# Kernel optimization log

Measured on AMD Instinct MI355X. Metric: run time of the kernel, lower is better.

Reference implementation:

```python
import jax, jax.numpy as jnp
import numpy as np

D_STATE = 16


def setup_inputs() -> dict:
    key = jax.random.key(0)
    ks = jax.random.split(key, 7)
    B, S, D = 8, 4096, 64
    ds = D_STATE
    x = jax.random.normal(ks[0], (B, S, D), dtype=jnp.float32)
    # Selection layers modeled as Linear(d_model, out). W_A scaled small so the
    # random transition matrices are contractive over 4096 steps.
    W_A = jax.random.normal(ks[1], (D, ds * ds), dtype=jnp.float32) * 0.01
    b_A = jnp.zeros((ds * ds,), dtype=jnp.float32)
    W_B = jax.random.normal(ks[2], (D, ds * D), dtype=jnp.float32) * 0.05
    b_B = jnp.zeros((ds * D,), dtype=jnp.float32)
    W_C = jax.random.normal(ks[3], (D, ds * D), dtype=jnp.float32) * 0.05
    b_C = jnp.zeros((ds * D,), dtype=jnp.float32)
    return {"x": x, "W_A": W_A, "b_A": b_A, "W_B": W_B, "b_B": b_B,
            "W_C": W_C, "b_C": b_C}


def reference(x, W_A, b_A, W_B, b_B, W_C, b_C):
    B, S, D = x.shape
    ds = D_STATE
    # Input-dependent (selective) parameters per timestep
    A = (x @ W_A + b_A).reshape(B, S, ds, ds)      # [B,S,ds,ds]
    Bm = (x @ W_B + b_B).reshape(B, S, ds, D)      # [B,S,ds,D]
    Cm = (x @ W_C + b_C).reshape(B, S, ds, D)      # [B,S,ds,D]
    # Pre-contract B_t @ x_t once: [B,S,ds]
    Bx = jnp.einsum('bsnd,bsd->bsn', Bm, x)

    def step(h, inputs):
        A_t, Bx_t = inputs                          # [B,ds,ds], [B,ds]
        h = jnp.einsum('bij,bj->bi', A_t, h) + Bx_t
        return h, h

    h0 = jnp.zeros((B, ds), dtype=x.dtype)
    _, hs = jax.lax.scan(step, h0,
                         (jnp.swapaxes(A, 0, 1), jnp.swapaxes(Bx, 0, 1)))
    hs = jnp.swapaxes(hs, 0, 1)                     # [B,S,ds]
    # output_t = C_t^T @ h_t  -> [B,S,D]
    return jnp.einsum('bsnd,bsn->bsd', Cm, hs)
```

## Files before the change

kernel.cpp:

```cpp
#include <hip/hip_runtime.h>

#define BATCH   8
#define SEQ     4096
#define DM      64
#define DS      16
#define BS      (BATCH*SEQ)
#define CHUNK   16
#define NCHT    (BS/CHUNK)
#define SG      16
#define NSG     (NCHT/SG)

typedef __attribute__((ext_vector_type(8))) __bf16 bf16x8;
typedef __attribute__((ext_vector_type(4))) float  f32x4;

__device__ __forceinline__ unsigned short f2bf(float f) {
  unsigned int u = __float_as_uint(f);
  u += 0x7fffu + ((u >> 16) & 1u);
  return (unsigned short)(u >> 16);
}
__device__ __forceinline__ float bflo(unsigned int u) { return __uint_as_float(u << 16); }
__device__ __forceinline__ float bfhi(unsigned int u) { return __uint_as_float(u & 0xffff0000u); }

#define AS_I 20
#define AS_T 324

__global__ __launch_bounds__(256) void k0_castw(
    const float* __restrict__ WA, const float* __restrict__ WB,
    const float* __restrict__ WC,
    unsigned short* __restrict__ WAt, unsigned short* __restrict__ WBt,
    unsigned short* __restrict__ WCt)
{
  const int o = blockIdx.x * 256 + threadIdx.x;
  if (o < 16384) {
    const int c = o >> 6, e = o & 63;
    WAt[o] = f2bf(WA[e * 256 + c]);
  } else if (o < 16384 + 65536) {
    const int p = o - 16384;
    const int c = p >> 6, e = p & 63;
    WBt[p] = f2bf(WB[e * 1024 + c]);
  } else {
    const int p = o - 16384 - 65536;
    const int c = p >> 6, e = p & 63;
    WCt[p] = f2bf(WC[e * 1024 + c]);
  }
}

__global__ __launch_bounds__(256, 1) void g1(
    const float* __restrict__ x, const unsigned short* __restrict__ WBt,
    const float* __restrict__ bB, const unsigned short* __restrict__ WAt,
    const float* __restrict__ bA, unsigned short* __restrict__ xb,
    unsigned short* __restrict__ Wt_ws, float* __restrict__ u_ws,
    float* __restrict__ P_ws, float* __restrict__ v_ws)
{
  __shared__ __align__(16) unsigned char smem[64 * AS_T * 2];
  float (*xs)[68]     = (float (*)[68])smem;
  float* bBs          = (float*)(smem + 17408);
  unsigned short* As  = (unsigned short*)smem;
  __shared__ __align__(16) float bxs[64][16];
  __shared__ __align__(16) float us[4][16];

  const int tid  = threadIdx.x;
  const int lane = tid & 63;
  const int l15  = lane & 15;
  const int quad = lane >> 4;
  const int w    = tid >> 6;
  const int t0   = blockIdx.x * 64;
  const int twl  = w * 16;

  {
    const float4* xg = (const float4*)(x + (size_t)t0 * DM);
    #pragma unroll
    for (int i = 0; i < 4; ++i) {
      const int f4 = tid + 256 * i;
      ((float4*)&xs[f4 >> 4][0])[f4 & 15] = xg[f4];
    }
    ((float4*)bBs)[tid] = ((const float4*)bB)[tid];
    if (tid < 64) us[tid >> 4][tid & 15] = 0.f;
  }
  __syncthreads();

  bf16x8 a0, a1;
  {
    const int row = twl + l15;
    union { bf16x8 v; ushort4 s[2]; } ua, ub;
    float4 p0 = *(const float4*)&xs[row][quad * 8];
    float4 p1 = *(const float4*)&xs[row][quad * 8 + 4];
    float4 p2 = *(const float4*)&xs[row][32 + quad * 8];
    float4 p3 = *(const float4*)&xs[row][32 + quad * 8 + 4];
    ua.s[0] = (ushort4){f2bf(p0.x), f2bf(p0.y), f2bf(p0.z), f2bf(p0.w)};
    ua.s[1] = (ushort4){f2bf(p1.x), f2bf(p1.y), f2bf(p1.z), f2bf(p1.w)};
    ub.s[0] = (ushort4){f2bf(p2.x), f2bf(p2.y), f2bf(p2.z), f2bf(p2.w)};
    ub.s[1] = (ushort4){f2bf(p3.x), f2bf(p3.y), f2bf(p3.z), f2bf(p3.w)};
    a0 = ua.v; a1 = ub.v;
    unsigned short* xp = xb + (size_t)(t0 + row) * 64 + quad * 8;
    *(bf16x8*)xp        = a0;
    *(bf16x8*)(xp + 32) = a1;
  }

  {
    bf16x8 wf[8];
    #pragma unroll
    for (int r = 0; r < 4; ++r) {
      const bf16x8* wv = (const bf16x8*)(WBt + (size_t)(r * 16 + l15) * 64);
      wf[2*r]   = wv[quad];
      wf[2*r+1] = wv[quad + 4];
    }
    #pragma unroll 1
    for (int n = 0; n < 16; ++n) {
      bf16x8 nf[8];
      if (n < 15) {
        #pragma unroll
        for (int r = 0; r < 4; ++r) {
          const bf16x8* wv = (const bf16x8*)(WBt + (size_t)(((n+1) * 4 + r) * 16 + l15) * 64);
          nf[2*r]   = wv[quad];
          nf[2*r+1] = wv[quad + 4];
        }
      }
      f32x4 ac[4];
      #pragma unroll
      for (int r = 0; r < 4; ++r) {
        f32x4 t = {0.f, 0.f, 0.f, 0.f};
        t = __builtin_amdgcn_mfma_f32_16x16x32_bf16(a0, wf[2*r],   t, 0, 0, 0);
        t = __builtin_amdgcn_mfma_f32_16x16x32_bf16(a1, wf[2*r+1], t, 0, 0, 0);
        ac[r] = t;
      }
      float part[4] = {0.f, 0.f, 0.f, 0.f};
      #pragma unroll
      for (int r = 0; r < 4; ++r) {
        const float bb = bBs[n * 64 + r * 16 + l15];
        #pragma unroll
        for (int reg = 0; reg < 4; ++reg) {
          const int tl = twl + quad * 4 + reg;
          part[reg] = fmaf(ac[r][reg] + bb, xs[tl][r * 16 + l15], part[reg]);
        }
      }
      #pragma unroll
      for (int off = 1; off < 16; off <<= 1) {
        #pragma unroll
        for (int reg = 0; reg < 4; ++reg)
          part[reg] += __shfl_xor(part[reg], off, 64);
      }
      if (l15 == 0) {
        #pragma unroll
        for (int reg = 0; reg < 4; ++reg)
          bxs[twl + quad * 4 + reg][n] = part[reg];
      }
      #pragma unroll
      for (int q = 0; q < 8; ++q) wf[q] = nf[q];
    }
  }
  __syncthreads();

  {
    bf16x8 c0, c1;
    {
      const bf16x8* wv = (const bf16x8*)(WAt + (size_t)(l15) * 64);
      c0 = wv[quad]; c1 = wv[quad + 4];
    }
    #pragma unroll 1
    for (int ns = 0; ns < 16; ++ns) {
      bf16x8 n0, n1;
      if (ns < 15) {
        const bf16x8* wv = (const bf16x8*)(WAt + (size_t)((ns+1) * 16 + l15) * 64);
        n0 = wv[quad]; n1 = wv[quad + 4];
      }
      f32x4 acc = {0.f, 0.f, 0.f, 0.f};
      acc = __builtin_amdgcn_mfma_f32_16x16x32_bf16(a0, c0, acc, 0, 0, 0);
      acc = __builtin_amdgcn_mfma_f32_16x16x32_bf16(a1, c1, acc, 0, 0, 0);
      const float bias = bA[ns * 16 + l15];
      #pragma unroll
      for (int r = 0; r < 4; ++r)
        As[(twl + quad * 4 + r) * AS_T + ns * AS_I + l15] = f2bf(acc[r] + bias);
      c0 = n0; c1 = n1;
    }
  }
  __syncthreads();

  {
    bf16x8 wb;
    #pragma unroll
    for (int j = 0; j < 8; ++j) wb[j] = (__bf16)((quad * 8 + j == l15) ? 1.f : 0.f);
    f32x4 d = {0.f, 0.f, 0.f, 0.f};
    const int qq = quad & 1;

    const unsigned short* rp = &As[twl * AS_T + l15 * AS_I];
    uint2 r0 = *(const uint2*)(rp);
    uint2 r1 = *(const uint2*)(rp + 4);
    uint2 r2 = *(const uint2*)(rp + 8);
    uint2 r3 = *(const uint2*)(rp + 12);

    #pragma unroll 1
    for (int t = 0; t < CHUNK; ++t) {
      const int tl = twl + t;

      uint4 abits;
      if (quad == 0)      abits = make_uint4(r0.x, r0.y, r1.x, r1.y);
      else if (quad == 1) abits = make_uint4(r2.x, r2.y, r3.x, r3.y);
      else                abits = make_uint4(0u, 0u, 0u, 0u);
      bf16x8 af = *(bf16x8*)&abits;

      uint2 p0, p1, p2, p3;
      if (t < CHUNK - 1) {
        const unsigned short* np = &As[(tl + 1) * AS_T + l15 * AS_I];
        p0 = *(const uint2*)(np);
        p1 = *(const uint2*)(np + 4);
        p2 = *(const uint2*)(np + 8);
        p3 = *(const uint2*)(np + 12);
      }

      f32x4 z4 = {0.f, 0.f, 0.f, 0.f};
      d = __builtin_amdgcn_mfma_f32_16x16x32_bf16(af, wb, z4, 0, 0, 0);

      float nu = bxs[tl][l15];
      {
        float4 U0 = *(const float4*)&us[w][0];
        float4 U1 = *(const float4*)&us[w][4];
        float4 U2 = *(const float4*)&us[w][8];
        float4 U3 = *(const float4*)&us[w][12];
        nu = fmaf(bflo(r0.x), U0.x, nu); nu = fmaf(bfhi(r0.x), U0.y, nu);
        nu = fmaf(bflo(r0.y), U0.z, nu); nu = fmaf(bfhi(r0.y), U0.w, nu);
        nu = fmaf(bflo(r1.x), U1.x, nu); nu = fmaf(bfhi(r1.x), U1.y, nu);
        nu = fmaf(bflo(r1.y), U1.z, nu); nu = fmaf(bfhi(r1.y), U1.w, nu);
        nu = fmaf(bflo(r2.x), U2.x, nu); nu = fmaf(bfhi(r2.x), U2.y, nu);
        nu = fmaf(bflo(r2.y), U2.z, nu); nu = fmaf(bfhi(r2.y), U2.w, nu);
        nu = fmaf(bflo(r3.x), U3.x, nu); nu = fmaf(bfhi(r3.x), U3.y, nu);
        nu = fmaf(bflo(r3.y), U3.z, nu); nu = fmaf(bfhi(r3.y), U3.w, nu);
      }

      bf16x8 nb;
      nb[0] = (__bf16)__shfl(d[0], (2 * qq + 0) * 16 + l15, 64);
      nb[1] = (__bf16)__shfl(d[1], (2 * qq + 0) * 16 + l15, 64);
      nb[2] = (__bf16)__shfl(d[2], (2 * qq + 0) * 16 + l15, 64);
      nb[3] = (__bf16)__shfl(d[3], (2 * qq + 0) * 16 + l15, 64);
      nb[4] = (__bf16)__shfl(d[0], (2 * qq + 1) * 16 + l15, 64);
      nb[5] = (__bf16)__shfl(d[1], (2 * qq + 1) * 16 + l15, 64);
      nb[6] = (__bf16)__shfl(d[2], (2 * qq + 1) * 16 + l15, 64);
      nb[7] = (__bf16)__shfl(d[3], (2 * qq + 1) * 16 + l15, 64);
      wb = nb;

      if (quad == 0) {
        us[w][l15] = nu;
        bxs[tl][l15] = nu;
      }
      #pragma unroll
      for (int r = 0; r < 4; ++r)
        As[tl * AS_T + (quad * 4 + r) * AS_I + l15] = f2bf(d[r]);

      r0 = p0; r1 = p1; r2 = p2; r3 = p3;
    }

    const int chunk = blockIdx.x * 4 + w;
    #pragma unroll
    for (int r = 0; r < 4; ++r)
      P_ws[(size_t)chunk * 256 + (quad * 4 + r) * 16 + l15] = d[r];
    if (quad == 0) v_ws[(size_t)chunk * DS + l15] = us[w][l15];
  }
  __syncthreads();

  {
    uint4* Wg = (uint4*)(Wt_ws + (size_t)t0 * 256);
    #pragma unroll 1
    for (int z = 0; z < 8; ++z) {
      const int p4 = z * 256 + tid;
      const int f  = p4 * 8;
      const int t  = f >> 8, i = (f >> 4) & 15, k = f & 15;
      const unsigned short* sp = &As[t * AS_T + i * AS_I + k];
      uint2 lo = *(const uint2*)(sp);
      uint2 hi = *(const uint2*)(sp + 4);
      Wg[p4] = make_uint4(lo.x, lo.y, hi.x, hi.y);
    }
    ((float4*)(u_ws + (size_t)t0 * DS))[tid] = ((const float4*)&bxs[0][0])[tid];
  }
}

__global__ __launch_bounds__(256) void k3a(
    const float* __restrict__ P_ws, const float* __restrict__ v_ws,
    float* __restrict__ Q_ws, float* __restrict__ w_ws)
{
  __shared__ float wsv[4][16];
  const int tid  = threadIdx.x;
  const int lane = tid & 63;
  const int l15  = lane & 15;
  const int quad = lane >> 4;
  const int wv   = tid >> 6;
  const int s    = blockIdx.x * 4 + wv;
  const int qq   = quad & 1;

  if (lane < 16) wsv[wv][lane] = 0.f;
  bf16x8 wb;
  #pragma unroll
  for (int j = 0; j < 8; ++j) wb[j] = (__bf16)((quad * 8 + j == l15) ? 1.f : 0.f);
  f32x4 d = {0.f, 0.f, 0.f, 0.f};

  #pragma unroll 1
  for (int t = 0; t < SG; ++t) {
    const int chunk = s * SG + t;
    float4 p0 = {0.f,0.f,0.f,0.f}, p1 = {0.f,0.f,0.f,0.f};
    if (quad < 2) {
      const float4* pr = (const float4*)(P_ws + (size_t)chunk * 256 + l15 * 16 + quad * 8);
      p0 = pr[0]; p1 = pr[1];
    }
    bf16x8 af;
    af[0] = (__bf16)p0.x; af[1] = (__bf16)p0.y; af[2] = (__bf16)p0.z; af[3] = (__bf16)p0.w;
    af[4] = (__bf16)p1.x; af[5] = (__bf16)p1.y; af[6] = (__bf16)p1.z; af[7] = (__bf16)p1.w;

    f32x4 z4 = {0.f, 0.f, 0.f, 0.f};
    d = __builtin_amdgcn_mfma_f32_16x16x32_bf16(af, wb, z4, 0, 0, 0);

    float part = 0.f;
    if (quad < 2) {
      const float* wrow = &wsv[wv][quad * 8];
      part = p0.x*wrow[0] + p0.y*wrow[1] + p0.z*wrow[2] + p0.w*wrow[3]
           + p1.x*wrow[4] + p1.y*wrow[5] + p1.z*wrow[6] + p1.w*wrow[7];
    }
    part += __shfl_xor(part, 16, 64);
    const float nv = v_ws[(size_t)chunk * DS + l15];

    bf16x8 nb;
    nb[0] = (__bf16)__shfl(d[0], (2 * qq + 0) * 16 + l15, 64);
    nb[1] = (__bf16)__shfl(d[1], (2 * qq + 0) * 16 + l15, 64);
    nb[2] = (__bf16)__shfl(d[2], (2 * qq + 0) * 16 + l15, 64);
    nb[3] = (__bf16)__shfl(d[3], (2 * qq + 0) * 16 + l15, 64);
    nb[4] = (__bf16)__shfl(d[0], (2 * qq + 1) * 16 + l15, 64);
    nb[5] = (__bf16)__shfl(d[1], (2 * qq + 1) * 16 + l15, 64);
    nb[6] = (__bf16)__shfl(d[2], (2 * qq + 1) * 16 + l15, 64);
    nb[7] = (__bf16)__shfl(d[3], (2 * qq + 1) * 16 + l15, 64);
    wb = nb;

    if (quad == 0) wsv[wv][l15] = part + nv;
  }

  #pragma unroll
  for (int r = 0; r < 4; ++r)
    Q_ws[(size_t)s * 256 + (quad * 4 + r) * 16 + l15] = d[r];
  if (quad == 0) w_ws[(size_t)s * DS + l15] = wsv[wv][l15];
}

__global__ __launch_bounds__(128) void k3b(
    const float* __restrict__ Q_ws, const float* __restrict__ w_ws,
    float* __restrict__ hbg_ws)
{
  const int tid = threadIdx.x;
  const int b = tid >> 4;
  const int r = tid & 15;
  float h = 0.f;

  #pragma unroll 1
  for (int g = 0; g < 16; ++g) {
    const int s = b * 16 + g;
    const float4* Pr = (const float4*)&Q_ws[(size_t)s * 256 + r * 16];
    float4 c0 = Pr[0], c1 = Pr[1], c2 = Pr[2], c3 = Pr[3];
    const float vc = w_ws[(size_t)s * DS + r];
    hbg_ws[(size_t)s * DS + r] = h;
    float acc = vc;
    acc += c0.x*__shfl(h, 0,16) + c0.y*__shfl(h, 1,16) + c0.z*__shfl(h, 2,16) + c0.w*__shfl(h, 3,16);
    acc += c1.x*__shfl(h, 4,16) + c1.y*__shfl(h, 5,16) + c1.z*__shfl(h, 6,16) + c1.w*__shfl(h, 7,16);
    acc += c2.x*__shfl(h, 8,16) + c2.y*__shfl(h, 9,16) + c2.z*__shfl(h,10,16) + c2.w*__shfl(h,11,16);
    acc += c3.x*__shfl(h,12,16) + c3.y*__shfl(h,13,16) + c3.z*__shfl(h,14,16) + c3.w*__shfl(h,15,16);
    h = acc;
  }
}

__global__ __launch_bounds__(256) void k3c(
    const float* __restrict__ P_ws, const float* __restrict__ v_ws,
    const float* __restrict__ hbg_ws, float* __restrict__ hb_ws)
{
  const int tid = threadIdx.x;
  const int s = blockIdx.x * 16 + (tid >> 4);
  const int r = tid & 15;
  float h = hbg_ws[(size_t)s * DS + r];

  #pragma unroll 1
  for (int t = 0; t < SG; ++t) {
    const int chunk = s * SG + t;
    const float4* Pr = (const float4*)&P_ws[(size_t)chunk * 256 + r * 16];
    float4 c0 = Pr[0], c1 = Pr[1], c2 = Pr[2], c3 = Pr[3];
    const float vc = v_ws[(size_t)chunk * DS + r];
    hb_ws[(size_t)chunk * DS + r] = h;
    float acc = vc;
    acc += c0.x*__shfl(h, 0,16) + c0.y*__shfl(h, 1,16) + c0.z*__shfl(h, 2,16) + c0.w*__shfl(h, 3,16);
    acc += c1.x*__shfl(h, 4,16) + c1.y*__shfl(h, 5,16) + c1.z*__shfl(h, 6,16) + c1.w*__shfl(h, 7,16);
    acc += c2.x*__shfl(h, 8,16) + c2.y*__shfl(h, 9,16) + c2.z*__shfl(h,10,16) + c2.w*__shfl(h,11,16);
    acc += c3.x*__shfl(h,12,16) + c3.y*__shfl(h,13,16) + c3.z*__shfl(h,14,16) + c3.w*__shfl(h,15,16);
    h = acc;
  }
}

__global__ __launch_bounds__(256, 1) void g2(
    const unsigned short* __restrict__ xb, const unsigned short* __restrict__ WCt,
    const float* __restrict__ bC, const unsigned short* __restrict__ Wt_ws,
    const float* __restrict__ u_ws, const float* __restrict__ hb_ws,
    float* __restrict__ out)
{
  __shared__ float hsh[64][17];
  __shared__ float bCs[1024];
  const int tid  = threadIdx.x;
  const int lane = tid & 63;
  const int l15  = lane & 15;
  const int quad = lane >> 4;
  const int w    = tid >> 6;
  const int t0   = blockIdx.x * 64;
  const int twl  = w * 16;

  ((float4*)bCs)[tid] = ((const float4*)bC)[tid];

  #pragma unroll
  for (int z = 0; z < 4; ++z) {
    const int gcell = z * 256 + tid;
    const int tl = gcell >> 4, i = gcell & 15;
    const int t = t0 + tl;
    const uint4* wr = (const uint4*)(Wt_ws + (size_t)t * 256 + i * 16);
    uint4 wa = wr[0], wbv = wr[1];
    const float4* hp = (const float4*)(hb_ws + (size_t)(t >> 4) * DS);
    float4 h0 = hp[0], h1 = hp[1], h2 = hp[2], h3 = hp[3];
    float acc = u_ws[(size_t)t * DS + i];
    acc = fmaf(bflo(wa.x),  h0.x, acc); acc = fmaf(bfhi(wa.x),  h0.y, acc);
    acc = fmaf(bflo(wa.y),  h0.z, acc); acc = fmaf(bfhi(wa.y),  h0.w, acc);
    acc = fmaf(bflo(wa.z),  h1.x, acc); acc = fmaf(bfhi(wa.z),  h1.y, acc);
    acc = fmaf(bflo(wa.w),  h1.z, acc); acc = fmaf(bfhi(wa.w),  h1.w, acc);
    acc = fmaf(bflo(wbv.x), h2.x, acc); acc = fmaf(bfhi(wbv.x), h2.y, acc);
    acc = fmaf(bflo(wbv.y), h2.z, acc); acc = fmaf(bfhi(wbv.y), h2.w, acc);
    acc = fmaf(bflo(wbv.z), h3.x, acc); acc = fmaf(bfhi(wbv.z), h3.y, acc);
    acc = fmaf(bflo(wbv.w), h3.z, acc); acc = fmaf(bfhi(wbv.w), h3.w, acc);
    hsh[tl][i] = acc;
  }

  const bf16x8* xv = (const bf16x8*)(xb + (size_t)(t0 + twl + l15) * 64);
  bf16x8 a0 = xv[quad];
  bf16x8 a1 = xv[quad + 4];
  __syncthreads();

  f32x4 ota[4];
  #pragma unroll
  for (int r = 0; r < 4; ++r) ota[r] = (f32x4){0.f, 0.f, 0.f, 0.f};

  {
    bf16x8 wf[8];
    #pragma unroll
    for (int r = 0; r < 4; ++r) {
      const bf16x8* wv = (const bf16x8*)(WCt + (size_t)(r * 16 + l15) * 64);
      wf[2*r]   = wv[quad];
      wf[2*r+1] = wv[quad + 4];
    }
    #pragma unroll 1
    for (int n = 0; n < 16; ++n) {
      bf16x8 nf[8];
      if (n < 15) {
        #pragma unroll
        for (int r = 0; r < 4; ++r) {
          const bf16x8* wv = (const bf16x8*)(WCt + (size_t)(((n+1) * 4 + r) * 16 + l15) * 64);
          nf[2*r]   = wv[quad];
          nf[2*r+1] = wv[quad + 4];
        }
      }
      f32x4 ac[4];
      #pragma unroll
      for (int r = 0; r < 4; ++r) {
        f32x4 t = {0.f, 0.f, 0.f, 0.f};
        t = __builtin_amdgcn_mfma_f32_16x16x32_bf16(a0, wf[2*r],   t, 0, 0, 0);
        t = __builtin_amdgcn_mfma_f32_16x16x32_bf16(a1, wf[2*r+1], t, 0, 0, 0);
        ac[r] = t;
      }
      float hn[4];
      #pragma unroll
      for (int reg = 0; reg < 4; ++reg) hn[reg] = hsh[twl + quad * 4 + reg][n];
      #pragma unroll
      for (int r = 0; r < 4; ++r) {
        const float bc = bCs[n * 64 + r * 16 + l15];
        #pragma unroll
        for (int reg = 0; reg < 4; ++reg)
          ota[r][reg] = fmaf(ac[r][reg] + bc, hn[reg], ota[r][reg]);
      }
      #pragma unroll
      for (int q = 0; q < 8; ++q) wf[q] = nf[q];
    }
  }

  #pragma unroll
  for (int r = 0; r < 4; ++r)
    #pragma unroll
    for (int reg = 0; reg < 4; ++reg)
      out[(size_t)(t0 + twl + quad * 4 + reg) * DM + r * 16 + l15] = ota[r][reg];
}

extern "C" void kernel_launch(void* const* d_in, const int* in_sizes, int n_in,
                              void* d_out, int out_size, void* d_ws, size_t ws_size,
                              hipStream_t stream) {
  const float* x  = (const float*)d_in[0];
  const float* WA = (const float*)d_in[1];
  const float* bA = (const float*)d_in[2];
  const float* WB = (const float*)d_in[3];
  const float* bB = (const float*)d_in[4];
  const float* WC = (const float*)d_in[5];
  const float* bC = (const float*)d_in[6];
  float* out = (float*)d_out;

  float* ws     = (float*)d_ws;
  float* P_ws   = ws;
  float* v_ws   = P_ws   + (size_t)NCHT * 256;
  float* u_ws   = v_ws   + (size_t)NCHT * DS;
  float* Q_ws   = u_ws   + (size_t)BS * DS;
  float* w_ws   = Q_ws   + (size_t)NSG * 256;
  float* hbg_ws = w_ws   + (size_t)NSG * DS;
  float* hb_ws  = hbg_ws + (size_t)NSG * DS;
  unsigned short* xb    = (unsigned short*)(hb_ws + (size_t)NCHT * DS);
  unsigned short* WAt   = xb  + (size_t)BS * 64;
  unsigned short* WBt   = WAt + 256 * 64;
  unsigned short* WCt   = WBt + 1024 * 64;
  unsigned short* Wt_ws = WCt + 1024 * 64;

  k0_castw<<<576,      256, 0, stream>>>(WA, WB, WC, WAt, WBt, WCt);
  g1      <<<BS / 64,  256, 0, stream>>>(x, WBt, bB, WAt, bA, xb, Wt_ws, u_ws, P_ws, v_ws);
  k3a     <<<NSG / 4,  256, 0, stream>>>(P_ws, v_ws, Q_ws, w_ws);
  k3b     <<<1,        128, 0, stream>>>(Q_ws, w_ws, hbg_ws);
  k3c     <<<NSG / 16, 256, 0, stream>>>(P_ws, v_ws, hbg_ws, hb_ws);
  g2      <<<BS / 64,  256, 0, stream>>>(xb, WCt, bC, Wt_ws, u_ws, hb_ws, out);
}
```

Baseline: 183.2 us.

## Split projection and chunk scan into separate kernels, raise occupancy, fuse k3b/k3c

Splits the old g1 into gAB, which computes the A and Bx projections over 32-token blocks with waves split across the state dimension, and gScan, which runs the per-chunk serial scan reading A from global memory. g2 also moves to 32-token blocks with waves split across output columns, and both use launch bounds allowing 4 blocks per CU. k3b and k3c are fused into one per-batch kernel that keeps the group boundary states in shared memory. The goal is more parallelism and occupancy and less serial work inside one big block, at the cost of an extra global round trip for the bf16 A matrices and Bx.

```diff
diff --git a/kernel.cpp b/kernel.cpp
--- a/kernel.cpp
+++ b/kernel.cpp
@@ -21,8 +21,7 @@
 __device__ __forceinline__ float bflo(unsigned int u) { return __uint_as_float(u << 16); }
 __device__ __forceinline__ float bfhi(unsigned int u) { return __uint_as_float(u & 0xffff0000u); }
 
-#define AS_I 20
-#define AS_T 324
+#define AS_R 264
 
 __global__ __launch_bounds__(256) void k0_castw(
     const float* __restrict__ WA, const float* __restrict__ WB,
@@ -45,37 +44,36 @@
   }
 }
 
-__global__ __launch_bounds__(256, 1) void g1(
+__global__ __launch_bounds__(256, 4) void gAB(
     const float* __restrict__ x, const unsigned short* __restrict__ WBt,
     const float* __restrict__ bB, const unsigned short* __restrict__ WAt,
     const float* __restrict__ bA, unsigned short* __restrict__ xb,
-    unsigned short* __restrict__ Wt_ws, float* __restrict__ u_ws,
-    float* __restrict__ P_ws, float* __restrict__ v_ws)
+    unsigned short* __restrict__ A_g, float* __restrict__ Bx_ws)
 {
-  __shared__ __align__(16) unsigned char smem[64 * AS_T * 2];
-  float (*xs)[68]     = (float (*)[68])smem;
-  float* bBs          = (float*)(smem + 17408);
-  unsigned short* As  = (unsigned short*)smem;
-  __shared__ __align__(16) float bxs[64][16];
-  __shared__ __align__(16) float us[4][16];
+  __shared__ __align__(16) unsigned char smem[32 * AS_R * 2];
+  float (*xs)[68]    = (float (*)[68])smem;
+  unsigned short* As = (unsigned short*)smem;
+  __shared__ __align__(16) float bBs[1024];
+  __shared__ __align__(16) float bxs[32][16];
 
   const int tid  = threadIdx.x;
   const int lane = tid & 63;
   const int l15  = lane & 15;
   const int quad = lane >> 4;
   const int w    = tid >> 6;
-  const int t0   = blockIdx.x * 64;
-  const int twl  = w * 16;
+  const int tsub = w & 1;
+  const int nh   = w >> 1;
+  const int t0   = blockIdx.x * 32;
+  const int twl  = tsub * 16;
 
   {
     const float4* xg = (const float4*)(x + (size_t)t0 * DM);
     #pragma unroll
-    for (int i = 0; i < 4; ++i) {
+    for (int i = 0; i < 2; ++i) {
       const int f4 = tid + 256 * i;
       ((float4*)&xs[f4 >> 4][0])[f4 & 15] = xg[f4];
     }
     ((float4*)bBs)[tid] = ((const float4*)bB)[tid];
-    if (tid < 64) us[tid >> 4][tid & 15] = 0.f;
   }
   __syncthreads();
 
@@ -92,29 +90,31 @@
     ub.s[0] = (ushort4){f2bf(p2.x), f2bf(p2.y), f2bf(p2.z), f2bf(p2.w)};
     ub.s[1] = (ushort4){f2bf(p3.x), f2bf(p3.y), f2bf(p3.z), f2bf(p3.w)};
     a0 = ua.v; a1 = ub.v;
-    unsigned short* xp = xb + (size_t)(t0 + row) * 64 + quad * 8;
-    *(bf16x8*)xp        = a0;
-    *(bf16x8*)(xp + 32) = a1;
+    if (w < 2) {
+      unsigned short* xp = xb + (size_t)(t0 + row) * 64 + quad * 8;
+      *(bf16x8*)xp        = a0;
+      *(bf16x8*)(xp + 32) = a1;
+    }
   }
 
   {
     bf16x8 wf[8];
     #pragma unroll
     for (int r = 0; r < 4; ++r) {
-      const bf16x8* wv = (const bf16x8*)(WBt + (size_t)(r * 16 + l15) * 64);
+      const bf16x8* wv = (const bf16x8*)(WBt + (size_t)(((nh * 8) * 4 + r) * 16 + l15) * 64);
       wf[2*r]   = wv[quad];
       wf[2*r+1] = wv[quad + 4];
     }
     #pragma unroll 1
-    for (int n = 0; n < 16; ++n) {
+    for (int nn = 0; nn < 8; ++nn) {
+      const int n  = nh * 8 + nn;
+      const int n2 = nh * 8 + ((nn + 1) & 7);
       bf16x8 nf[8];
-      if (n < 15) {
-        #pragma unroll
-        for (int r = 0; r < 4; ++r) {
-          const bf16x8* wv = (const bf16x8*)(WBt + (size_t)(((n+1) * 4 + r) * 16 + l15) * 64);
-          nf[2*r]   = wv[quad];
-          nf[2*r+1] = wv[quad + 4];
-        }
+      #pragma unroll
+      for (int r = 0; r < 4; ++r) {
+        const bf16x8* wv = (const bf16x8*)(WBt + (size_t)((n2 * 4 + r) * 16 + l15) * 64);
+        nf[2*r]   = wv[quad];
+        nf[2*r+1] = wv[quad + 4];
       }
       f32x4 ac[4];
       #pragma unroll
@@ -154,14 +154,16 @@
   {
     bf16x8 c0, c1;
     {
-      const bf16x8* wv = (const bf16x8*)(WAt + (size_t)(l15) * 64);
+      const bf16x8* wv = (const bf16x8*)(WAt + (size_t)((nh * 8) * 16 + l15) * 64);
       c0 = wv[quad]; c1 = wv[quad + 4];
     }
     #pragma unroll 1
-    for (int ns = 0; ns < 16; ++ns) {
+    for (int nsn = 0; nsn < 8; ++nsn) {
+      const int ns  = nh * 8 + nsn;
+      const int ns2 = nh * 8 + ((nsn + 1) & 7);
       bf16x8 n0, n1;
-      if (ns < 15) {
-        const bf16x8* wv = (const bf16x8*)(WAt + (size_t)((ns+1) * 16 + l15) * 64);
+      {
+        const bf16x8* wv = (const bf16x8*)(WAt + (size_t)(ns2 * 16 + l15) * 64);
         n0 = wv[quad]; n1 = wv[quad + 4];
       }
       f32x4 acc = {0.f, 0.f, 0.f, 0.f};
@@ -170,107 +172,125 @@
       const float bias = bA[ns * 16 + l15];
       #pragma unroll
       for (int r = 0; r < 4; ++r)
-        As[(twl + quad * 4 + r) * AS_T + ns * AS_I + l15] = f2bf(acc[r] + bias);
+        As[(twl + quad * 4 + r) * AS_R + ns * 16 + l15] = f2bf(acc[r] + bias);
       c0 = n0; c1 = n1;
     }
   }
   __syncthreads();
 
   {
-    bf16x8 wb;
+    uint4* Ag4 = (uint4*)(A_g + (size_t)t0 * 256);
     #pragma unroll
-    for (int j = 0; j < 8; ++j) wb[j] = (__bf16)((quad * 8 + j == l15) ? 1.f : 0.f);
-    f32x4 d = {0.f, 0.f, 0.f, 0.f};
-    const int qq = quad & 1;
-
-    const unsigned short* rp = &As[twl * AS_T + l15 * AS_I];
-    uint2 r0 = *(const uint2*)(rp);
-    uint2 r1 = *(const uint2*)(rp + 4);
-    uint2 r2 = *(const uint2*)(rp + 8);
-    uint2 r3 = *(const uint2*)(rp + 12);
-
-    #pragma unroll 1
-    for (int t = 0; t < CHUNK; ++t) {
-      const int tl = twl + t;
-
-      uint4 abits;
-      if (quad == 0)      abits = make_uint4(r0.x, r0.y, r1.x, r1.y);
-      else if (quad == 1) abits = make_uint4(r2.x, r2.y, r3.x, r3.y);
-      else                abits = make_uint4(0u, 0u, 0u, 0u);
-      bf16x8 af = *(bf16x8*)&abits;
-
-      uint2 p0, p1, p2, p3;
-      if (t < CHUNK - 1) {
-        const unsigned short* np = &As[(tl + 1) * AS_T + l15 * AS_I];
-        p0 = *(const uint2*)(np);
-        p1 = *(const uint2*)(np + 4);
-        p2 = *(const uint2*)(np + 8);
-        p3 = *(const uint2*)(np + 12);
-      }
-
-      f32x4 z4 = {0.f, 0.f, 0.f, 0.f};
-      d = __builtin_amdgcn_mfma_f32_16x16x32_bf16(af, wb, z4, 0, 0, 0);
-
-      float nu = bxs[tl][l15];
-      {
-        float4 U0 = *(const float4*)&us[w][0];
-        float4 U1 = *(const float4*)&us[w][4];
-        float4 U2 = *(const float4*)&us[w][8];
-        float4 U3 = *(const float4*)&us[w][12];
-        nu = fmaf(bflo(r0.x), U0.x, nu); nu = fmaf(bfhi(r0.x), U0.y, nu);
-        nu = fmaf(bflo(r0.y), U0.z, nu); nu = fmaf(bfhi(r0.y), U0.w, nu);
-        nu = fmaf(bflo(r1.x), U1.x, nu); nu = fmaf(bfhi(r1.x), U1.y, nu);
-        nu = fmaf(bflo(r1.y), U1.z, nu); nu = fmaf(bfhi(r1.y), U1.w, nu);
-        nu = fmaf(bflo(r2.x), U2.x, nu); nu = fmaf(bfhi(r2.x), U2.y, nu);
-        nu = fmaf(bflo(r2.y), U2.z, nu); nu = fmaf(bfhi(r2.y), U2.w, nu);
-        nu = fmaf(bflo(r3.x), U3.x, nu); nu = fmaf(bfhi(r3.x), U3.y, nu);
-        nu = fmaf(bflo(r3.y), U3.z, nu); nu = fmaf(bfhi(r3.y), U3.w, nu);
-      }
-
-      bf16x8 nb;
-      nb[0] = (__bf16)__shfl(d[0], (2 * qq + 0) * 16 + l15, 64);
-      nb[1] = (__bf16)__shfl(d[1], (2 * qq + 0) * 16 + l15, 64);
-      nb[2] = (__bf16)__shfl(d[2], (2 * qq + 0) * 16 + l15, 64);
-      nb[3] = (__bf16)__shfl(d[3], (2 * qq + 0) * 16 + l15, 64);
-      nb[4] = (__bf16)__shfl(d[0], (2 * qq + 1) * 16 + l15, 64);
-      nb[5] = (__bf16)__shfl(d[1], (2 * qq + 1) * 16 + l15, 64);
-      nb[6] = (__bf16)__shfl(d[2], (2 * qq + 1) * 16 + l15, 64);
-      nb[7] = (__bf16)__shfl(d[3], (2 * qq + 1) * 16 + l15, 64);
-      wb = nb;
-
-      if (quad == 0) {
-        us[w][l15] = nu;
-        bxs[tl][l15] = nu;
-      }
-      #pragma unroll
-      for (int r = 0; r < 4; ++r)
-        As[tl * AS_T + (quad * 4 + r) * AS_I + l15] = f2bf(d[r]);
-
-      r0 = p0; r1 = p1; r2 = p2; r3 = p3;
-    }
-
-    const int chunk = blockIdx.x * 4 + w;
+    for (int z = 0; z < 4; ++z) {
+      const int p4 = z * 256 + tid;
+      const int f  = p4 * 8;
+      const int t  = f >> 8, rem = f & 255;
+      const unsigned short* sp = &As[t * AS_R + rem];
+      uint2 lo = *(const uint2*)sp;
+      uint2 hi = *(const uint2*)(sp + 4);
+      Ag4[p4] = make_uint4(lo.x, lo.y, hi.x, hi.y);
+    }
+    if (tid < 128)
+      ((float4*)(Bx_ws + (size_t)t0 * DS))[tid] = ((const float4*)&bxs[0][0])[tid];
+  }
+}
+
+__global__ __launch_bounds__(256) void gScan(
+    const unsigned short* __restrict__ A_g, const float* __restrict__ Bx_ws,
+    unsigned short* __restrict__ Wt_ws, float* __restrict__ u_ws,
+    float* __restrict__ P_ws, float* __restrict__ v_ws)
+{
+  __shared__ __align__(16) float us4[4][16];
+  const int tid  = threadIdx.x;
+  const int lane = tid & 63;
+  const int l15  = lane & 15;
+  const int quad = lane >> 4;
+  const int w    = tid >> 6;
+  const int c    = blockIdx.x * 4 + w;
+  const int tbase = c * CHUNK;
+  const int qq   = quad & 1;
+
+  if (lane < 16) us4[w][lane] = 0.f;
+
+  bf16x8 wb;
+  #pragma unroll
+  for (int j = 0; j < 8; ++j) wb[j] = (__bf16)((quad * 8 + j == l15) ? 1.f : 0.f);
+  f32x4 d = {0.f, 0.f, 0.f, 0.f};
+
+  const unsigned short* Ab = A_g + (size_t)tbase * 256;
+  uint2 r0, r1, r2, r3;
+  {
+    const unsigned short* rp = Ab + l15 * 16;
+    r0 = *(const uint2*)(rp);
+    r1 = *(const uint2*)(rp + 4);
+    r2 = *(const uint2*)(rp + 8);
+    r3 = *(const uint2*)(rp + 12);
+  }
+  float bx = Bx_ws[(size_t)tbase * DS + l15];
+
+  #pragma unroll 1
+  for (int t = 0; t < CHUNK; ++t) {
+    uint2 p0, p1, p2, p3; float bxn = 0.f;
+    if (t < CHUNK - 1) {
+      const unsigned short* np = Ab + (t + 1) * 256 + l15 * 16;
+      p0 = *(const uint2*)(np);
+      p1 = *(const uint2*)(np + 4);
+      p2 = *(const uint2*)(np + 8);
+      p3 = *(const uint2*)(np + 12);
+      bxn = Bx_ws[(size_t)(tbase + t + 1) * DS + l15];
+    }
+
+    uint4 abits;
+    if (quad == 0)      abits = make_uint4(r0.x, r0.y, r1.x, r1.y);
+    else if (quad == 1) abits = make_uint4(r2.x, r2.y, r3.x, r3.y);
+    else                abits = make_uint4(0u, 0u, 0u, 0u);
+    bf16x8 af = *(bf16x8*)&abits;
+
+    f32x4 z4 = {0.f, 0.f, 0.f, 0.f};
+    d = __builtin_amdgcn_mfma_f32_16x16x32_bf16(af, wb, z4, 0, 0, 0);
+
+    float nu = bx;
+    {
+      float4 U0 = *(const float4*)&us4[w][0];
+      float4 U1 = *(const float4*)&us4[w][4];
+      float4 U2 = *(const float4*)&us4[w][8];
+      float4 U3 = *(const float4*)&us4[w][12];
+      nu = fmaf(bflo(r0.x), U0.x, nu); nu = fmaf(bfhi(r0.x), U0.y, nu);
+      nu = fmaf(bflo(r0.y), U0.z, nu); nu = fmaf(bfhi(r0.y), U0.w, nu);
+      nu = fmaf(bflo(r1.x), U1.x, nu); nu = fmaf(bfhi(r1.x), U1.y, nu);
+      nu = fmaf(bflo(r1.y), U1.z, nu); nu = fmaf(bfhi(r1.y), U1.w, nu);
+      nu = fmaf(bflo(r2.x), U2.x, nu); nu = fmaf(bfhi(r2.x), U2.y, nu);
+      nu = fmaf(bflo(r2.y), U2.z, nu); nu = fmaf(bfhi(r2.y), U2.w, nu);
+      nu = fmaf(bflo(r3.x), U3.x, nu); nu = fmaf(bfhi(r3.x), U3.y, nu);
+      nu = fmaf(bflo(r3.y), U3.z, nu); nu = fmaf(bfhi(r3.y), U3.w, nu);
+    }
+
+    bf16x8 nb;
+    nb[0] = (__bf16)__shfl(d[0], (2 * qq + 0) * 16 + l15, 64);
+    nb[1] = (__bf16)__shfl(d[1], (2 * qq + 0) * 16 + l15, 64);
+    nb[2] = (__bf16)__shfl(d[2], (2 * qq + 0) * 16 + l15, 64);
+    nb[3] = (__bf16)__shfl(d[3], (2 * qq + 0) * 16 + l15, 64);
+    nb[4] = (__bf16)__shfl(d[0], (2 * qq + 1) * 16 + l15, 64);
+    nb[5] = (__bf16)__shfl(d[1], (2 * qq + 1) * 16 + l15, 64);
+    nb[6] = (__bf16)__shfl(d[2], (2 * qq + 1) * 16 + l15, 64);
+    nb[7] = (__bf16)__shfl(d[3], (2 * qq + 1) * 16 + l15, 64);
+    wb = nb;
+
+    if (quad == 0) {
+      us4[w][l15] = nu;
+      u_ws[(size_t)(tbase + t) * DS + l15] = nu;
+    }
     #pragma unroll
     for (int r = 0; r < 4; ++r)
-      P_ws[(size_t)chunk * 256 + (quad * 4 + r) * 16 + l15] = d[r];
-    if (quad == 0) v_ws[(size_t)chunk * DS + l15] = us[w][l15];
-  }
-  __syncthreads();
-
-  {
-    uint4* Wg = (uint4*)(Wt_ws + (size_t)t0 * 256);
-    #pragma unroll 1
-    for (int z = 0; z < 8; ++z) {
-      const int p4 = z * 256 + tid;
-      const int f  = p4 * 8;
-      const int t  = f >> 8, i = (f >> 4) & 15, k = f & 15;
-      const unsigned short* sp = &As[t * AS_T + i * AS_I + k];
-      uint2 lo = *(const uint2*)(sp);
-      uint2 hi = *(const uint2*)(sp + 4);
-      Wg[p4] = make_uint4(lo.x, lo.y, hi.x, hi.y);
-    }
-    ((float4*)(u_ws + (size_t)t0 * DS))[tid] = ((const float4*)&bxs[0][0])[tid];
-  }
+      Wt_ws[(size_t)(tbase + t) * 256 + (quad * 4 + r) * 16 + l15] = f2bf(d[r]);
+
+    r0 = p0; r1 = p1; r2 = p2; r3 = p3; bx = bxn;
+  }
+
+  #pragma unroll
+  for (int r = 0; r < 4; ++r)
+    P_ws[(size_t)c * 256 + (quad * 4 + r) * 16 + l15] = d[r];
+  if (quad == 0) v_ws[(size_t)c * DS + l15] = us4[w][l15];
 }
 
 __global__ __launch_bounds__(256) void k3a(
@@ -336,40 +356,39 @@
   if (quad == 0) w_ws[(size_t)s * DS + l15] = wsv[wv][l15];
 }
 
-__global__ __launch_bounds__(128) void k3b(
+__global__ __launch_bounds__(256) void k3bc(
     const float* __restrict__ Q_ws, const float* __restrict__ w_ws,
-    float* __restrict__ hbg_ws)
+    const float* __restrict__ P_ws, const float* __restrict__ v_ws,
+    float* __restrict__ hb_ws)
 {
+  __shared__ float hbgs[16][16];
   const int tid = threadIdx.x;
-  const int b = tid >> 4;
+  const int b   = blockIdx.x;
+
+  if (tid < 16) {
+    const int r = tid;
+    float h = 0.f;
+    #pragma unroll 1
+    for (int g = 0; g < 16; ++g) {
+      const int s = b * 16 + g;
+      const float4* Pr = (const float4*)&Q_ws[(size_t)s * 256 + r * 16];
+      float4 c0 = Pr[0], c1 = Pr[1], c2 = Pr[2], c3 = Pr[3];
+      const float vc = w_ws[(size_t)s * DS + r];
+      hbgs[g][r] = h;
+      float acc = vc;
+      acc += c0.x*__shfl(h, 0,16) + c0.y*__shfl(h, 1,16) + c0.z*__shfl(h, 2,16) + c0.w*__shfl(h, 3,16);
+      acc += c1.x*__shfl(h, 4,16) + c1.y*__shfl(h, 5,16) + c1.z*__shfl(h, 6,16) + c1.w*__shfl(h, 7,16);
+      acc += c2.x*__shfl(h, 8,16) + c2.y*__shfl(h, 9,16) + c2.z*__shfl(h,10,16) + c2.w*__shfl(h,11,16);
+      acc += c3.x*__shfl(h,12,16) + c3.y*__shfl(h,13,16) + c3.z*__shfl(h,14,16) + c3.w*__shfl(h,15,16);
+      h = acc;
+    }
+  }
+  __syncthreads();
+
+  const int g = tid >> 4;
   const int r = tid & 15;
-  float h = 0.f;
-
-  #pragma unroll 1
-  for (int g = 0; g < 16; ++g) {
-    const int s = b * 16 + g;
-    const float4* Pr = (const float4*)&Q_ws[(size_t)s * 256 + r * 16];
-    float4 c0 = Pr[0], c1 = Pr[1], c2 = Pr[2], c3 = Pr[3];
-    const float vc = w_ws[(size_t)s * DS + r];
-    hbg_ws[(size_t)s * DS + r] = h;
-    float acc = vc;
-    acc += c0.x*__shfl(h, 0,16) + c0.y*__shfl(h, 1,16) + c0.z*__shfl(h, 2,16) + c0.w*__shfl(h, 3,16);
-    acc += c1.x*__shfl(h, 4,16) + c1.y*__shfl(h, 5,16) + c1.z*__shfl(h, 6,16) + c1.w*__shfl(h, 7,16);
-    acc += c2.x*__shfl(h, 8,16) + c2.y*__shfl(h, 9,16) + c2.z*__shfl(h,10,16) + c2.w*__shfl(h,11,16);
-    acc += c3.x*__shfl(h,12,16) + c3.y*__shfl(h,13,16) + c3.z*__shfl(h,14,16) + c3.w*__shfl(h,15,16);
-    h = acc;
-  }
-}
-
-__global__ __launch_bounds__(256) void k3c(
-    const float* __restrict__ P_ws, const float* __restrict__ v_ws,
-    const float* __restrict__ hbg_ws, float* __restrict__ hb_ws)
-{
-  const int tid = threadIdx.x;
-  const int s = blockIdx.x * 16 + (tid >> 4);
-  const int r = tid & 15;
-  float h = hbg_ws[(size_t)s * DS + r];
-
+  const int s = b * 16 + g;
+  float h = hbgs[g][r];
   #pragma unroll 1
   for (int t = 0; t < SG; ++t) {
     const int chunk = s * SG + t;
@@ -386,26 +405,28 @@
   }
 }
 
-__global__ __launch_bounds__(256, 1) void g2(
+__global__ __launch_bounds__(256, 4) void g2(
     const unsigned short* __restrict__ xb, const unsigned short* __restrict__ WCt,
     const float* __restrict__ bC, const unsigned short* __restrict__ Wt_ws,
     const float* __restrict__ u_ws, const float* __restrict__ hb_ws,
     float* __restrict__ out)
 {
-  __shared__ float hsh[64][17];
+  __shared__ float hsh[32][17];
   __shared__ float bCs[1024];
   const int tid  = threadIdx.x;
   const int lane = tid & 63;
   const int l15  = lane & 15;
   const int quad = lane >> 4;
   const int w    = tid >> 6;
-  const int t0   = blockIdx.x * 64;
-  const int twl  = w * 16;
+  const int tsub = w & 1;
+  const int dh   = w >> 1;
+  const int t0   = blockIdx.x * 32;
+  const int twl  = tsub * 16;
 
   ((float4*)bCs)[tid] = ((const float4*)bC)[tid];
 
   #pragma unroll
-  for (int z = 0; z < 4; ++z) {
+  for (int z = 0; z < 2; ++z) {
     const int gcell = z * 256 + tid;
     const int tl = gcell >> 4, i = gcell & 15;
     const int t = t0 + tl;
@@ -430,57 +451,61 @@
   bf16x8 a1 = xv[quad + 4];
   __syncthreads();
 
-  f32x4 ota[4];
-  #pragma unroll
-  for (int r = 0; r < 4; ++r) ota[r] = (f32x4){0.f, 0.f, 0.f, 0.f};
-
-  {
-    bf16x8 wf[8];
+  f32x4 ota[2];
+  ota[0] = (f32x4){0.f, 0.f, 0.f, 0.f};
+  ota[1] = (f32x4){0.f, 0.f, 0.f, 0.f};
+
+  {
+    bf16x8 wf[4];
     #pragma unroll
-    for (int r = 0; r < 4; ++r) {
+    for (int rr = 0; rr < 2; ++rr) {
+      const int r = dh * 2 + rr;
       const bf16x8* wv = (const bf16x8*)(WCt + (size_t)(r * 16 + l15) * 64);
-      wf[2*r]   = wv[quad];
-      wf[2*r+1] = wv[quad + 4];
+      wf[2*rr]   = wv[quad];
+      wf[2*rr+1] = wv[quad + 4];
     }
     #pragma unroll 1
     for (int n = 0; n < 16; ++n) {
-      bf16x8 nf[8];
-      if (n < 15) {
-        #pragma unroll
-        for (int r = 0; r < 4; ++r) {
-          const bf16x8* wv = (const bf16x8*)(WCt + (size_t)(((n+1) * 4 + r) * 16 + l15) * 64);
-          nf[2*r]   = wv[quad];
-          nf[2*r+1] = wv[quad + 4];
-        }
-      }
-      f32x4 ac[4];
-      #pragma unroll
-      for (int r = 0; r < 4; ++r) {
+      const int n2 = (n + 1) & 15;
+      bf16x8 nf[4];
+      #pragma unroll
+      for (int rr = 0; rr < 2; ++rr) {
+        const int r = dh * 2 + rr;
+        const bf16x8* wv = (const bf16x8*)(WCt + (size_t)((n2 * 4 + r) * 16 + l15) * 64);
+        nf[2*rr]   = wv[quad];
+        nf[2*rr+1] = wv[quad + 4];
+      }
+      f32x4 ac[2];
+      #pragma unroll
+      for (int rr = 0; rr < 2; ++rr) {
         f32x4 t = {0.f, 0.f, 0.f, 0.f};
-        t = __builtin_amdgcn_mfma_f32_16x16x32_bf16(a0, wf[2*r],   t, 0, 0, 0);
-        t = __builtin_amdgcn_mfma_f32_16x16x32_bf16(a1, wf[2*r+1], t, 0, 0, 0);
-        ac[r] = t;
+        t = __builtin_amdgcn_mfma_f32_16x16x32_bf16(a0, wf[2*rr],   t, 0, 0, 0);
+        t = __builtin_amdgcn_mfma_f32_16x16x32_bf16(a1, wf[2*rr+1], t, 0, 0, 0);
+        ac[rr] = t;
       }
       float hn[4];
       #pragma unroll
       for (int reg = 0; reg < 4; ++reg) hn[reg] = hsh[twl + quad * 4 + reg][n];
       #pragma unroll
-      for (int r = 0; r < 4; ++r) {
+      for (int rr = 0; rr < 2; ++rr) {
+        const int r = dh * 2 + rr;
         const float bc = bCs[n * 64 + r * 16 + l15];
         #pragma unroll
         for (int reg = 0; reg < 4; ++reg)
-          ota[r][reg] = fmaf(ac[r][reg] + bc, hn[reg], ota[r][reg]);
-      }
-      #pragma unroll
-      for (int q = 0; q < 8; ++q) wf[q] = nf[q];
+          ota[rr][reg] = fmaf(ac[rr][reg] + bc, hn[reg], ota[rr][reg]);
+      }
+      #pragma unroll
+      for (int q = 0; q < 4; ++q) wf[q] = nf[q];
     }
   }
 
   #pragma unroll
-  for (int r = 0; r < 4; ++r)
+  for (int rr = 0; rr < 2; ++rr) {
+    const int r = dh * 2 + rr;
     #pragma unroll
     for (int reg = 0; reg < 4; ++reg)
-      out[(size_t)(t0 + twl + quad * 4 + reg) * DM + r * 16 + l15] = ota[r][reg];
+      out[(size_t)(t0 + twl + quad * 4 + reg) * DM + r * 16 + l15] = ota[rr][reg];
+  }
 }
 
 extern "C" void kernel_launch(void* const* d_in, const int* in_sizes, int n_in,
@@ -501,18 +526,19 @@
   float* u_ws   = v_ws   + (size_t)NCHT * DS;
   float* Q_ws   = u_ws   + (size_t)BS * DS;
   float* w_ws   = Q_ws   + (size_t)NSG * 256;
-  float* hbg_ws = w_ws   + (size_t)NSG * DS;
-  float* hb_ws  = hbg_ws + (size_t)NSG * DS;
-  unsigned short* xb    = (unsigned short*)(hb_ws + (size_t)NCHT * DS);
+  float* hb_ws  = w_ws   + (size_t)NSG * DS;
+  float* Bx_ws  = hb_ws  + (size_t)NCHT * DS;
+  unsigned short* xb    = (unsigned short*)(Bx_ws + (size_t)BS * DS);
   unsigned short* WAt   = xb  + (size_t)BS * 64;
   unsigned short* WBt   = WAt + 256 * 64;
   unsigned short* WCt   = WBt + 1024 * 64;
-  unsigned short* Wt_ws = WCt + 1024 * 64;
+  unsigned short* A_g   = WCt + 1024 * 64;
+  unsigned short* Wt_ws = A_g + (size_t)BS * 256;
 
   k0_castw<<<576,      256, 0, stream>>>(WA, WB, WC, WAt, WBt, WCt);
-  g1      <<<BS / 64,  256, 0, stream>>>(x, WBt, bB, WAt, bA, xb, Wt_ws, u_ws, P_ws, v_ws);
+  gAB     <<<BS / 32,  256, 0, stream>>>(x, WBt, bB, WAt, bA, xb, A_g, Bx_ws);
+  gScan   <<<NCHT / 4, 256, 0, stream>>>(A_g, Bx_ws, Wt_ws, u_ws, P_ws, v_ws);
   k3a     <<<NSG / 4,  256, 0, stream>>>(P_ws, v_ws, Q_ws, w_ws);
-  k3b     <<<1,        128, 0, stream>>>(Q_ws, w_ws, hbg_ws);
-  k3c     <<<NSG / 16, 256, 0, stream>>>(P_ws, v_ws, hbg_ws, hb_ws);
-  g2      <<<BS / 64,  256, 0, stream>>>(xb, WCt, bC, Wt_ws, u_ws, hb_ws, out);
-}
+  k3bc    <<<BATCH,    256, 0, stream>>>(Q_ws, w_ws, P_ws, v_ws, hb_ws);
+  g2      <<<BS / 32,  256, 0, stream>>>(xb, WCt, bC, Wt_ws, u_ws, hb_ws, out);
+}
```

Result: slower. 194.1 us (+6.0%).

## Fuse scan-carry kernels per batch and split g2 output columns across waves

Applied to the files above, without the earlier changes.

Merges k3b and k3c into one kernel with one block per batch. Each block runs the 16-step supergroup carry in a single 16-lane group, keeps the carries in shared memory, then propagates them to its chunks. This removes one launch and the hbg global round trip. g2 now handles 32 timesteps per block, with wave pairs splitting the 64 output columns, and raises occupancy to 4 blocks per CU to double the grid and cut per-wave register use. The cost is more redundant loads of x and W_C across waves, plus an unconditional wrapped prefetch on the last iteration.

```diff
diff --git a/kernel.cpp b/kernel.cpp
--- a/kernel.cpp
+++ b/kernel.cpp
@@ -336,40 +336,39 @@
   if (quad == 0) w_ws[(size_t)s * DS + l15] = wsv[wv][l15];
 }
 
-__global__ __launch_bounds__(128) void k3b(
+__global__ __launch_bounds__(256) void k3bc(
     const float* __restrict__ Q_ws, const float* __restrict__ w_ws,
-    float* __restrict__ hbg_ws)
+    const float* __restrict__ P_ws, const float* __restrict__ v_ws,
+    float* __restrict__ hb_ws)
 {
+  __shared__ float hbgs[16][16];
   const int tid = threadIdx.x;
-  const int b = tid >> 4;
+  const int b   = blockIdx.x;
+
+  if (tid < 16) {
+    const int r = tid;
+    float h = 0.f;
+    #pragma unroll 1
+    for (int g = 0; g < 16; ++g) {
+      const int s = b * 16 + g;
+      const float4* Pr = (const float4*)&Q_ws[(size_t)s * 256 + r * 16];
+      float4 c0 = Pr[0], c1 = Pr[1], c2 = Pr[2], c3 = Pr[3];
+      const float vc = w_ws[(size_t)s * DS + r];
+      hbgs[g][r] = h;
+      float acc = vc;
+      acc += c0.x*__shfl(h, 0,16) + c0.y*__shfl(h, 1,16) + c0.z*__shfl(h, 2,16) + c0.w*__shfl(h, 3,16);
+      acc += c1.x*__shfl(h, 4,16) + c1.y*__shfl(h, 5,16) + c1.z*__shfl(h, 6,16) + c1.w*__shfl(h, 7,16);
+      acc += c2.x*__shfl(h, 8,16) + c2.y*__shfl(h, 9,16) + c2.z*__shfl(h,10,16) + c2.w*__shfl(h,11,16);
+      acc += c3.x*__shfl(h,12,16) + c3.y*__shfl(h,13,16) + c3.z*__shfl(h,14,16) + c3.w*__shfl(h,15,16);
+      h = acc;
+    }
+  }
+  __syncthreads();
+
+  const int g = tid >> 4;
   const int r = tid & 15;
-  float h = 0.f;
-
-  #pragma unroll 1
-  for (int g = 0; g < 16; ++g) {
-    const int s = b * 16 + g;
-    const float4* Pr = (const float4*)&Q_ws[(size_t)s * 256 + r * 16];
-    float4 c0 = Pr[0], c1 = Pr[1], c2 = Pr[2], c3 = Pr[3];
-    const float vc = w_ws[(size_t)s * DS + r];
-    hbg_ws[(size_t)s * DS + r] = h;
-    float acc = vc;
-    acc += c0.x*__shfl(h, 0,16) + c0.y*__shfl(h, 1,16) + c0.z*__shfl(h, 2,16) + c0.w*__shfl(h, 3,16);
-    acc += c1.x*__shfl(h, 4,16) + c1.y*__shfl(h, 5,16) + c1.z*__shfl(h, 6,16) + c1.w*__shfl(h, 7,16);
-    acc += c2.x*__shfl(h, 8,16) + c2.y*__shfl(h, 9,16) + c2.z*__shfl(h,10,16) + c2.w*__shfl(h,11,16);
-    acc += c3.x*__shfl(h,12,16) + c3.y*__shfl(h,13,16) + c3.z*__shfl(h,14,16) + c3.w*__shfl(h,15,16);
-    h = acc;
-  }
-}
-
-__global__ __launch_bounds__(256) void k3c(
-    const float* __restrict__ P_ws, const float* __restrict__ v_ws,
-    const float* __restrict__ hbg_ws, float* __restrict__ hb_ws)
-{
-  const int tid = threadIdx.x;
-  const int s = blockIdx.x * 16 + (tid >> 4);
-  const int r = tid & 15;
-  float h = hbg_ws[(size_t)s * DS + r];
-
+  const int s = b * 16 + g;
+  float h = hbgs[g][r];
   #pragma unroll 1
   for (int t = 0; t < SG; ++t) {
     const int chunk = s * SG + t;
@@ -386,26 +385,28 @@
   }
 }
 
-__global__ __launch_bounds__(256, 1) void g2(
+__global__ __launch_bounds__(256, 4) void g2(
     const unsigned short* __restrict__ xb, const unsigned short* __restrict__ WCt,
     const float* __restrict__ bC, const unsigned short* __restrict__ Wt_ws,
     const float* __restrict__ u_ws, const float* __restrict__ hb_ws,
     float* __restrict__ out)
 {
-  __shared__ float hsh[64][17];
+  __shared__ float hsh[32][17];
   __shared__ float bCs[1024];
   const int tid  = threadIdx.x;
   const int lane = tid & 63;
   const int l15  = lane & 15;
   const int quad = lane >> 4;
   const int w    = tid >> 6;
-  const int t0   = blockIdx.x * 64;
-  const int twl  = w * 16;
+  const int tsub = w & 1;
+  const int dh   = w >> 1;
+  const int t0   = blockIdx.x * 32;
+  const int twl  = tsub * 16;
 
   ((float4*)bCs)[tid] = ((const float4*)bC)[tid];
 
   #pragma unroll
-  for (int z = 0; z < 4; ++z) {
+  for (int z = 0; z < 2; ++z) {
     const int gcell = z * 256 + tid;
     const int tl = gcell >> 4, i = gcell & 15;
     const int t = t0 + tl;
@@ -430,57 +431,61 @@
   bf16x8 a1 = xv[quad + 4];
   __syncthreads();
 
-  f32x4 ota[4];
-  #pragma unroll
-  for (int r = 0; r < 4; ++r) ota[r] = (f32x4){0.f, 0.f, 0.f, 0.f};
-
-  {
-    bf16x8 wf[8];
+  f32x4 ota[2];
+  ota[0] = (f32x4){0.f, 0.f, 0.f, 0.f};
+  ota[1] = (f32x4){0.f, 0.f, 0.f, 0.f};
+
+  {
+    bf16x8 wf[4];
     #pragma unroll
-    for (int r = 0; r < 4; ++r) {
+    for (int rr = 0; rr < 2; ++rr) {
+      const int r = dh * 2 + rr;
       const bf16x8* wv = (const bf16x8*)(WCt + (size_t)(r * 16 + l15) * 64);
-      wf[2*r]   = wv[quad];
-      wf[2*r+1] = wv[quad + 4];
+      wf[2*rr]   = wv[quad];
+      wf[2*rr+1] = wv[quad + 4];
     }
     #pragma unroll 1
     for (int n = 0; n < 16; ++n) {
-      bf16x8 nf[8];
-      if (n < 15) {
-        #pragma unroll
-        for (int r = 0; r < 4; ++r) {
-          const bf16x8* wv = (const bf16x8*)(WCt + (size_t)(((n+1) * 4 + r) * 16 + l15) * 64);
-          nf[2*r]   = wv[quad];
-          nf[2*r+1] = wv[quad + 4];
-        }
-      }
-      f32x4 ac[4];
-      #pragma unroll
-      for (int r = 0; r < 4; ++r) {
+      const int n2 = (n + 1) & 15;
+      bf16x8 nf[4];
+      #pragma unroll
+      for (int rr = 0; rr < 2; ++rr) {
+        const int r = dh * 2 + rr;
+        const bf16x8* wv = (const bf16x8*)(WCt + (size_t)((n2 * 4 + r) * 16 + l15) * 64);
+        nf[2*rr]   = wv[quad];
+        nf[2*rr+1] = wv[quad + 4];
+      }
+      f32x4 ac[2];
+      #pragma unroll
+      for (int rr = 0; rr < 2; ++rr) {
         f32x4 t = {0.f, 0.f, 0.f, 0.f};
-        t = __builtin_amdgcn_mfma_f32_16x16x32_bf16(a0, wf[2*r],   t, 0, 0, 0);
-        t = __builtin_amdgcn_mfma_f32_16x16x32_bf16(a1, wf[2*r+1], t, 0, 0, 0);
-        ac[r] = t;
+        t = __builtin_amdgcn_mfma_f32_16x16x32_bf16(a0, wf[2*rr],   t, 0, 0, 0);
+        t = __builtin_amdgcn_mfma_f32_16x16x32_bf16(a1, wf[2*rr+1], t, 0, 0, 0);
+        ac[rr] = t;
       }
       float hn[4];
       #pragma unroll
       for (int reg = 0; reg < 4; ++reg) hn[reg] = hsh[twl + quad * 4 + reg][n];
       #pragma unroll
-      for (int r = 0; r < 4; ++r) {
+      for (int rr = 0; rr < 2; ++rr) {
+        const int r = dh * 2 + rr;
         const float bc = bCs[n * 64 + r * 16 + l15];
         #pragma unroll
         for (int reg = 0; reg < 4; ++reg)
-          ota[r][reg] = fmaf(ac[r][reg] + bc, hn[reg], ota[r][reg]);
-      }
-      #pragma unroll
-      for (int q = 0; q < 8; ++q) wf[q] = nf[q];
+          ota[rr][reg] = fmaf(ac[rr][reg] + bc, hn[reg], ota[rr][reg]);
+      }
+      #pragma unroll
+      for (int q = 0; q < 4; ++q) wf[q] = nf[q];
     }
   }
 
   #pragma unroll
-  for (int r = 0; r < 4; ++r)
+  for (int rr = 0; rr < 2; ++rr) {
+    const int r = dh * 2 + rr;
     #pragma unroll
     for (int reg = 0; reg < 4; ++reg)
-      out[(size_t)(t0 + twl + quad * 4 + reg) * DM + r * 16 + l15] = ota[r][reg];
+      out[(size_t)(t0 + twl + quad * 4 + reg) * DM + r * 16 + l15] = ota[rr][reg];
+  }
 }
 
 extern "C" void kernel_launch(void* const* d_in, const int* in_sizes, int n_in,
@@ -501,18 +506,16 @@
   float* u_ws   = v_ws   + (size_t)NCHT * DS;
   float* Q_ws   = u_ws   + (size_t)BS * DS;
   float* w_ws   = Q_ws   + (size_t)NSG * 256;
-  float* hbg_ws = w_ws   + (size_t)NSG * DS;
-  float* hb_ws  = hbg_ws + (size_t)NSG * DS;
+  float* hb_ws  = w_ws   + (size_t)NSG * DS;
   unsigned short* xb    = (unsigned short*)(hb_ws + (size_t)NCHT * DS);
   unsigned short* WAt   = xb  + (size_t)BS * 64;
   unsigned short* WBt   = WAt + 256 * 64;
   unsigned short* WCt   = WBt + 1024 * 64;
   unsigned short* Wt_ws = WCt + 1024 * 64;
 
-  k0_castw<<<576,      256, 0, stream>>>(WA, WB, WC, WAt, WBt, WCt);
-  g1      <<<BS / 64,  256, 0, stream>>>(x, WBt, bB, WAt, bA, xb, Wt_ws, u_ws, P_ws, v_ws);
-  k3a     <<<NSG / 4,  256, 0, stream>>>(P_ws, v_ws, Q_ws, w_ws);
-  k3b     <<<1,        128, 0, stream>>>(Q_ws, w_ws, hbg_ws);
-  k3c     <<<NSG / 16, 256, 0, stream>>>(P_ws, v_ws, hbg_ws, hb_ws);
-  g2      <<<BS / 64,  256, 0, stream>>>(xb, WCt, bC, Wt_ws, u_ws, hb_ws, out);
-}
+  k0_castw<<<576,     256, 0, stream>>>(WA, WB, WC, WAt, WBt, WCt);
+  g1      <<<BS / 64, 256, 0, stream>>>(x, WBt, bB, WAt, bA, xb, Wt_ws, u_ws, P_ws, v_ws);
+  k3a     <<<NSG / 4, 256, 0, stream>>>(P_ws, v_ws, Q_ws, w_ws);
+  k3bc    <<<BATCH,   256, 0, stream>>>(Q_ws, w_ws, P_ws, v_ws, hb_ws);
+  g2      <<<BS / 32, 256, 0, stream>>>(xb, WCt, bC, Wt_ws, u_ws, hb_ws, out);
+}
```

After: 183.7 us. About the same (+0.3%).
